# Kernel tuning notes

Hardware: AMD Instinct MI355X
Metric: run time of the kernel (lower is better)

The kernel has to match this reference:

```python
import jax, jax.numpy as jnp
import numpy as np

C_IN = 128
C_QK = C_IN // 8


def setup_inputs() -> dict:
    key = jax.random.key(0)
    kx, kq, kk, kv = jax.random.split(key, 4)
    x = jax.random.normal(kx, (8, C_IN, 64, 64), dtype=jnp.float32)
    # 1x1 conv weights, stored as (c_out, c_in); fan-in scaled init
    s = 1.0 / np.sqrt(C_IN)
    Wq = jax.random.normal(kq, (C_QK, C_IN), dtype=jnp.float32) * s
    Wk = jax.random.normal(kk, (C_QK, C_IN), dtype=jnp.float32) * s
    Wv = jax.random.normal(kv, (C_IN, C_IN), dtype=jnp.float32) * s
    gamma = jnp.ones((1,), dtype=jnp.float32) * 0.5  # nonzero so residual branch matters
    return {"x": x, "Wq": Wq, "Wk": Wk, "Wv": Wv, "gamma": gamma}


def reference(x, Wq, Wk, Wv, gamma):
    b, c, h, w = x.shape
    xt = rearr = x.reshape(b, c, h * w)            # b c n
    q = jnp.einsum('oc,bcn->bno', Wq, xt)          # b n c//8
    k = jnp.einsum('oc,bcn->bon', Wk, xt)          # b c//8 n
    v = jnp.einsum('oc,bcn->bno', Wv, xt)          # b n c
    energy = jnp.einsum('bno,bom->bnm', q, k)      # b n n (no scale, per source)
    attn = jax.nn.softmax(energy, axis=-1)
    out = jnp.einsum('bnm,bmc->bnc', attn, v)      # b n c
    out = out.transpose(0, 2, 1).reshape(b, c, h, w)
    return x + gamma[0] * out
```

## Files before the change

### kernel.cpp

```cpp
#include <hip/hip_runtime.h>
#include <hip/hip_bf16.h>


typedef __bf16 bf16x8 __attribute__((ext_vector_type(8)));
typedef __bf16 bf16x4 __attribute__((ext_vector_type(4)));
typedef float  f32x16 __attribute__((ext_vector_type(16)));

static constexpr int Bb = 8, Cc = 128, Nn = 4096, CQ = 16;

__device__ __forceinline__ f32x16 mfma32(bf16x8 a, bf16x8 b, f32x16 c) {
    return __builtin_amdgcn_mfma_f32_32x32x16_bf16(a, b, c, 0, 0, 0);
}
struct HL { __bf16 h, l; };
__device__ __forceinline__ HL hilo(float f) {
    HL r;
    r.h = (__bf16)f;
    r.l = (__bf16)(f - (float)r.h);
    return r;
}

__global__ __launch_bounds__(384) void qkv_kernel(
    const float* __restrict__ x, const float* __restrict__ Wq,
    const float* __restrict__ Wk, const float* __restrict__ Wv,
    __bf16* __restrict__ qw, __bf16* __restrict__ kw, __bf16* __restrict__ vw)
{
    const int b = blockIdx.y, tb = blockIdx.x, n0 = tb * 64, t = threadIdx.x;
    const int wave = t >> 6, lane = t & 63, lr = lane & 31, lq = lane >> 5;

    __shared__ __bf16 xh[64][136], xl[64][136];
    __shared__ __bf16 sc[4][32][40];

    if (t < 256) {
        const int n = lane, ci0 = (t >> 6) * 32;
        #pragma unroll
        for (int g = 0; g < 4; ++g) {
            float v[8];
            #pragma unroll
            for (int k = 0; k < 8; ++k)
                v[k] = x[((size_t)(b * Cc + ci0 + g * 8 + k)) * Nn + n0 + n];
            bf16x8 h8, l8;
            #pragma unroll
            for (int k = 0; k < 8; ++k) { HL z = hilo(v[k]); h8[k] = z.h; l8[k] = z.l; }
            *(bf16x8*)&xh[n][ci0 + g * 8] = h8;
            *(bf16x8*)&xl[n][ci0 + g * 8] = l8;
        }
    }
    __syncthreads();

    if (wave < 2) {
        const int nh = wave;
        const float* wrow = (lr < 16) ? (Wq + (size_t)lr * Cc)
                                      : (Wk + (size_t)(lr - 16) * Cc);
        f32x16 acc = {};
        #pragma unroll
        for (int ks = 0; ks < 8; ++ks) {
            float4 w0 = *(const float4*)(wrow + ks * 16 + lq * 8);
            float4 w1 = *(const float4*)(wrow + ks * 16 + lq * 8 + 4);
            bf16x8 ah, al;
            HL z;
            z = hilo(w0.x); ah[0] = z.h; al[0] = z.l;
            z = hilo(w0.y); ah[1] = z.h; al[1] = z.l;
            z = hilo(w0.z); ah[2] = z.h; al[2] = z.l;
            z = hilo(w0.w); ah[3] = z.h; al[3] = z.l;
            z = hilo(w1.x); ah[4] = z.h; al[4] = z.l;
            z = hilo(w1.y); ah[5] = z.h; al[5] = z.l;
            z = hilo(w1.z); ah[6] = z.h; al[6] = z.l;
            z = hilo(w1.w); ah[7] = z.h; al[7] = z.l;
            bf16x8 bh = *(const bf16x8*)&xh[nh * 32 + lr][ks * 16 + lq * 8];
            bf16x8 bl = *(const bf16x8*)&xl[nh * 32 + lr][ks * 16 + lq * 8];
            acc = mfma32(ah, bh, acc);
            acc = mfma32(al, bh, acc);
            acc = mfma32(ah, bl, acc);
        }
        const int tile = tb * 2 + nh;
        __bf16* qb = qw + (((size_t)b * 128 + tile) << 10);
        __bf16* kb = kw + (((size_t)b * 128 + tile) << 10);
        #pragma unroll
        for (int rg = 0; rg < 4; ++rg) {
            bf16x4 h4, l4;
            #pragma unroll
            for (int j = 0; j < 4; ++j) {
                float v = acc[rg * 4 + j];
                if (rg < 2) v *= 1.44269504089f;
                HL z = hilo(v);
                h4[j] = z.h; l4[j] = z.l;
            }
            const int off = (rg & 1) * 256 + lr * 8 + 4 * lq;
            __bf16* base = (rg < 2) ? qb : kb;
            *(bf16x4*)(base + off) = h4;
            *(bf16x4*)(base + 512 + off) = l4;
        }
    } else {
        const int ct = wave - 2;
        const int klr = (lr & ~12) | ((lr & 4) << 1) | ((lr & 8) >> 1);
        for (int nh = 0; nh < 2; ++nh) {
            f32x16 acc = {};
            #pragma unroll
            for (int ks = 0; ks < 8; ++ks) {
                const float* wp = Wv + (size_t)(ct * 32 + lr) * Cc + ks * 16 + lq * 8;
                float4 w0 = *(const float4*)wp;
                float4 w1 = *(const float4*)(wp + 4);
                bf16x8 a = { (__bf16)w0.x, (__bf16)w0.y, (__bf16)w0.z, (__bf16)w0.w,
                             (__bf16)w1.x, (__bf16)w1.y, (__bf16)w1.z, (__bf16)w1.w };
                bf16x8 bh = *(const bf16x8*)&xh[nh * 32 + lr][ks * 16 + lq * 8];
                acc = mfma32(a, bh, acc);
            }
            #pragma unroll
            for (int r = 0; r < 16; ++r) {
                int crow = (r & 3) + 8 * (r >> 2) + 4 * lq;
                sc[ct][crow][klr] = (__bf16)acc[r];
            }
            const int chunk = tb * 2 + nh;
            __bf16* vb = vw + (((size_t)b * 128 + chunk) << 12) + ct * 1024;
            #pragma unroll
            for (int u = 0; u < 2; ++u) {
                bf16x8 row = *(const bf16x8*)&sc[ct][lr][u * 16 + lq * 8];
                *(bf16x8*)(vb + u * 512 + lane * 8) = row;
            }
        }
    }
}

__global__ __launch_bounds__(256, 2) void attn_kernel(
    const float* __restrict__ x, const __bf16* __restrict__ qw,
    const __bf16* __restrict__ kw, const __bf16* __restrict__ vw,
    const float* __restrict__ gamma, float* __restrict__ out)
{
    const int h = blockIdx.x;
    const int b = h & 7;
    const int qt = h >> 3;
    const int t = threadIdx.x;
    const int wave = t >> 6, lane = t & 63, lr = lane & 31, lq = lane >> 5;
    const int kr = wave;

    __shared__ float accbuf[32][129];
    __shared__ float lbuf[32];

    const __bf16* qb = qw + (((size_t)b * 128 + qt) << 10) + lane * 8;
    const bf16x8 qhi = *(const bf16x8*)qb;
    const bf16x8 qlo = *(const bf16x8*)(qb + 512);

    const int c0 = kr * 32;
    const __bf16* kp = kw + (((size_t)b * 128 + c0) << 10) + lane * 8;
    const __bf16* vp = vw + (((size_t)b * 128 + c0) << 12) + lane * 8;

    f32x16 acc[4] = {{}, {}, {}, {}};
    float l_part = 0.f;

    bf16x8 akh = *(const bf16x8*)kp, akl = *(const bf16x8*)(kp + 512);
    bf16x8 av[8], bv[8];
    #pragma unroll
    for (int u = 0; u < 8; ++u) av[u] = *(const bf16x8*)(vp + u * 512);
    bf16x8 bkh, bkl;

    auto body = [&](const bf16x8& Kh, const bf16x8& Kl, const bf16x8 (&V)[8]) {
        f32x16 s = {};
        __builtin_amdgcn_s_setprio(1);
        s = mfma32(Kh, qhi, s);
        s = mfma32(Kl, qhi, s);
        s = mfma32(Kh, qlo, s);
        __builtin_amdgcn_s_setprio(0);

        float p[16];
        #pragma unroll
        for (int r = 0; r < 16; ++r) p[r] = __builtin_amdgcn_exp2f(s[r]);
        l_part += ((((p[0] + p[1]) + (p[2] + p[3])) + ((p[4] + p[5]) + (p[6] + p[7])))
                 + (((p[8] + p[9]) + (p[10] + p[11])) + ((p[12] + p[13]) + (p[14] + p[15]))));

        bf16x8 F0, F1;
        #pragma unroll
        for (int j = 0; j < 8; ++j) {
            F0[j] = (__bf16)p[j];
            F1[j] = (__bf16)p[8 + j];
        }

        __builtin_amdgcn_s_setprio(1);
        #pragma unroll
        for (int ct = 0; ct < 4; ++ct) {
            acc[ct] = mfma32(V[2 * ct],     F0, acc[ct]);
            acc[ct] = mfma32(V[2 * ct + 1], F1, acc[ct]);
        }
        __builtin_amdgcn_s_setprio(0);
    };

    for (int it = 0; it < 15; ++it) {
        kp += 1024; vp += 4096;
        bkh = *(const bf16x8*)kp; bkl = *(const bf16x8*)(kp + 512);
        #pragma unroll
        for (int u = 0; u < 8; ++u) bv[u] = *(const bf16x8*)(vp + u * 512);
        body(akh, akl, av);
        kp += 1024; vp += 4096;
        akh = *(const bf16x8*)kp; akl = *(const bf16x8*)(kp + 512);
        #pragma unroll
        for (int u = 0; u < 8; ++u) av[u] = *(const bf16x8*)(vp + u * 512);
        body(bkh, bkl, bv);
    }
    kp += 1024; vp += 4096;
    bkh = *(const bf16x8*)kp; bkl = *(const bf16x8*)(kp + 512);
    #pragma unroll
    for (int u = 0; u < 8; ++u) bv[u] = *(const bf16x8*)(vp + u * 512);
    body(akh, akl, av);
    body(bkh, bkl, bv);

    l_part += __shfl_xor(l_part, 32);

    if (kr == 0) {
        #pragma unroll
        for (int ct = 0; ct < 4; ++ct)
            #pragma unroll
            for (int r = 0; r < 16; ++r) {
                int c = (r & 3) + 8 * (r >> 2) + 4 * lq + 32 * ct;
                accbuf[lr][c] = acc[ct][r];
            }
        if (lane < 32) lbuf[lr] = l_part;
    }
    __syncthreads();
    if (kr != 0) {
        #pragma unroll
        for (int ct = 0; ct < 4; ++ct)
            #pragma unroll
            for (int r = 0; r < 16; ++r) {
                int c = (r & 3) + 8 * (r >> 2) + 4 * lq + 32 * ct;
                atomicAdd(&accbuf[lr][c], acc[ct][r]);
            }
        if (lane < 32) atomicAdd(&lbuf[lr], l_part);
    }
    __syncthreads();

    const float g = gamma[0];
    const int q = t & 31, cg = t >> 5;
    const float linv = 1.0f / lbuf[q];
    const int n0b = qt * 32;
    #pragma unroll
    for (int i = 0; i < 16; ++i) {
        int c = cg + 8 * i;
        size_t idx = ((size_t)(b * Cc + c)) * Nn + n0b + q;
        out[idx] = x[idx] + g * accbuf[q][c] * linv;
    }
}

extern "C" void kernel_launch(void* const* d_in, const int* in_sizes, int n_in,
                              void* d_out, int out_size, void* d_ws, size_t ws_size,
                              hipStream_t stream) {
    const float* x  = (const float*)d_in[0];
    const float* Wq = (const float*)d_in[1];
    const float* Wk = (const float*)d_in[2];
    const float* Wv = (const float*)d_in[3];
    const float* gm = (const float*)d_in[4];

    __bf16* qw = (__bf16*)d_ws;
    __bf16* kw = qw + (size_t)Bb * 128 * 1024;
    __bf16* vw = kw + (size_t)Bb * 128 * 1024;

    qkv_kernel<<<dim3(Nn / 64, Bb), 384, 0, stream>>>(x, Wq, Wk, Wv, qw, kw, vw);
    attn_kernel<<<dim3(Nn / 32 * Bb), 256, 0, stream>>>(x, qw, kw, vw, gm,
                                                        (float*)d_out);
}
```

Measured before the change: 187.4 us.

## Use persistent 512-thread attention blocks processing four query tiles each

The attention kernel now launches 256 blocks of 512 threads (one per CU) instead of 1024 blocks of 256 threads. Each block has two 4-wave halves, and each half handles two query tiles in sequence, reducing its partial results through a doubled shared-memory buffer. The aim is to cut block launch and tail overhead and to let the two halves share K/V reads through cache. The cost is fewer waves in flight per CU and extra block-wide barriers between tiles.

Result: slower. 213.1 us (+13.7%).

```diff
diff --git a/kernel.cpp b/kernel.cpp
--- a/kernel.cpp
+++ b/kernel.cpp
@@ -121,121 +121,133 @@
     }
 }
 
-__global__ __launch_bounds__(256, 2) void attn_kernel(
+__global__ __launch_bounds__(512, 2) void attn_kernel(
     const float* __restrict__ x, const __bf16* __restrict__ qw,
     const __bf16* __restrict__ kw, const __bf16* __restrict__ vw,
     const float* __restrict__ gamma, float* __restrict__ out)
 {
-    const int h = blockIdx.x;
-    const int b = h & 7;
-    const int qt = h >> 3;
+    const int i = blockIdx.x;
+    const int b = i & 7;
+    const int qt0 = (i >> 3) * 4;
     const int t = threadIdx.x;
     const int wave = t >> 6, lane = t & 63, lr = lane & 31, lq = lane >> 5;
-    const int kr = wave;
-
-    __shared__ float accbuf[32][129];
-    __shared__ float lbuf[32];
-
-    const __bf16* qb = qw + (((size_t)b * 128 + qt) << 10) + lane * 8;
-    const bf16x8 qhi = *(const bf16x8*)qb;
-    const bf16x8 qlo = *(const bf16x8*)(qb + 512);
-
+    const int kr = wave & 3, hh = wave >> 2;
+
+    __shared__ float accbuf[2][32][129];
+    __shared__ float lbuf[2][32];
+
+    const float g = gamma[0];
+    const __bf16* kwb = kw + (((size_t)b * 128) << 10);
+    const __bf16* vwb = vw + (((size_t)b * 128) << 12);
     const int c0 = kr * 32;
-    const __bf16* kp = kw + (((size_t)b * 128 + c0) << 10) + lane * 8;
-    const __bf16* vp = vw + (((size_t)b * 128 + c0) << 12) + lane * 8;
-
-    f32x16 acc[4] = {{}, {}, {}, {}};
-    float l_part = 0.f;
-
-    bf16x8 akh = *(const bf16x8*)kp, akl = *(const bf16x8*)(kp + 512);
-    bf16x8 av[8], bv[8];
-    #pragma unroll
-    for (int u = 0; u < 8; ++u) av[u] = *(const bf16x8*)(vp + u * 512);
-    bf16x8 bkh, bkl;
-
-    auto body = [&](const bf16x8& Kh, const bf16x8& Kl, const bf16x8 (&V)[8]) {
-        f32x16 s = {};
-        __builtin_amdgcn_s_setprio(1);
-        s = mfma32(Kh, qhi, s);
-        s = mfma32(Kl, qhi, s);
-        s = mfma32(Kh, qlo, s);
-        __builtin_amdgcn_s_setprio(0);
-
-        float p[16];
-        #pragma unroll
-        for (int r = 0; r < 16; ++r) p[r] = __builtin_amdgcn_exp2f(s[r]);
-        l_part += ((((p[0] + p[1]) + (p[2] + p[3])) + ((p[4] + p[5]) + (p[6] + p[7])))
-                 + (((p[8] + p[9]) + (p[10] + p[11])) + ((p[12] + p[13]) + (p[14] + p[15]))));
-
-        bf16x8 F0, F1;
-        #pragma unroll
-        for (int j = 0; j < 8; ++j) {
-            F0[j] = (__bf16)p[j];
-            F1[j] = (__bf16)p[8 + j];
-        }
-
-        __builtin_amdgcn_s_setprio(1);
-        #pragma unroll
-        for (int ct = 0; ct < 4; ++ct) {
-            acc[ct] = mfma32(V[2 * ct],     F0, acc[ct]);
-            acc[ct] = mfma32(V[2 * ct + 1], F1, acc[ct]);
-        }
-        __builtin_amdgcn_s_setprio(0);
-    };
-
-    for (int it = 0; it < 15; ++it) {
+
+    for (int u = 0; u < 2; ++u) {
+        const int qt = qt0 + u * 2 + hh;
+
+        const __bf16* qb = qw + (((size_t)b * 128 + qt) << 10) + lane * 8;
+        const bf16x8 qhi = *(const bf16x8*)qb;
+        const bf16x8 qlo = *(const bf16x8*)(qb + 512);
+
+        const __bf16* kp = kwb + ((size_t)c0 << 10) + lane * 8;
+        const __bf16* vp = vwb + ((size_t)c0 << 12) + lane * 8;
+
+        f32x16 acc[4] = {{}, {}, {}, {}};
+        float l_part = 0.f;
+
+        bf16x8 akh = *(const bf16x8*)kp, akl = *(const bf16x8*)(kp + 512);
+        bf16x8 av[8], bv[8];
+        #pragma unroll
+        for (int v8 = 0; v8 < 8; ++v8) av[v8] = *(const bf16x8*)(vp + v8 * 512);
+        bf16x8 bkh, bkl;
+
+        auto body = [&](const bf16x8& Kh, const bf16x8& Kl, const bf16x8 (&V)[8]) {
+            f32x16 s = {};
+            __builtin_amdgcn_s_setprio(1);
+            s = mfma32(Kh, qhi, s);
+            s = mfma32(Kl, qhi, s);
+            s = mfma32(Kh, qlo, s);
+            __builtin_amdgcn_s_setprio(0);
+
+            float p[16];
+            #pragma unroll
+            for (int r = 0; r < 16; ++r) p[r] = __builtin_amdgcn_exp2f(s[r]);
+            l_part += ((((p[0] + p[1]) + (p[2] + p[3])) + ((p[4] + p[5]) + (p[6] + p[7])))
+                     + (((p[8] + p[9]) + (p[10] + p[11])) + ((p[12] + p[13]) + (p[14] + p[15]))));
+
+            bf16x8 F0, F1;
+            #pragma unroll
+            for (int j = 0; j < 8; ++j) {
+                F0[j] = (__bf16)p[j];
+                F1[j] = (__bf16)p[8 + j];
+            }
+
+            __builtin_amdgcn_s_setprio(1);
+            #pragma unroll
+            for (int ct = 0; ct < 4; ++ct) {
+                acc[ct] = mfma32(V[2 * ct],     F0, acc[ct]);
+                acc[ct] = mfma32(V[2 * ct + 1], F1, acc[ct]);
+            }
+            __builtin_amdgcn_s_setprio(0);
+        };
+
+        for (int it = 0; it < 15; ++it) {
+            kp += 1024; vp += 4096;
+            bkh = *(const bf16x8*)kp; bkl = *(const bf16x8*)(kp + 512);
+            #pragma unroll
+            for (int v8 = 0; v8 < 8; ++v8) bv[v8] = *(const bf16x8*)(vp + v8 * 512);
+            body(akh, akl, av);
+            kp += 1024; vp += 4096;
+            akh = *(const bf16x8*)kp; akl = *(const bf16x8*)(kp + 512);
+            #pragma unroll
+            for (int v8 = 0; v8 < 8; ++v8) av[v8] = *(const bf16x8*)(vp + v8 * 512);
+            body(bkh, bkl, bv);
+        }
         kp += 1024; vp += 4096;
         bkh = *(const bf16x8*)kp; bkl = *(const bf16x8*)(kp + 512);
         #pragma unroll
-        for (int u = 0; u < 8; ++u) bv[u] = *(const bf16x8*)(vp + u * 512);
+        for (int v8 = 0; v8 < 8; ++v8) bv[v8] = *(const bf16x8*)(vp + v8 * 512);
         body(akh, akl, av);
-        kp += 1024; vp += 4096;
-        akh = *(const bf16x8*)kp; akl = *(const bf16x8*)(kp + 512);
-        #pragma unroll
-        for (int u = 0; u < 8; ++u) av[u] = *(const bf16x8*)(vp + u * 512);
         body(bkh, bkl, bv);
-    }
-    kp += 1024; vp += 4096;
-    bkh = *(const bf16x8*)kp; bkl = *(const bf16x8*)(kp + 512);
-    #pragma unroll
-    for (int u = 0; u < 8; ++u) bv[u] = *(const bf16x8*)(vp + u * 512);
-    body(akh, akl, av);
-    body(bkh, bkl, bv);
-
-    l_part += __shfl_xor(l_part, 32);
-
-    if (kr == 0) {
-        #pragma unroll
-        for (int ct = 0; ct < 4; ++ct)
-            #pragma unroll
-            for (int r = 0; r < 16; ++r) {
-                int c = (r & 3) + 8 * (r >> 2) + 4 * lq + 32 * ct;
-                accbuf[lr][c] = acc[ct][r];
-            }
-        if (lane < 32) lbuf[lr] = l_part;
-    }
-    __syncthreads();
-    if (kr != 0) {
-        #pragma unroll
-        for (int ct = 0; ct < 4; ++ct)
-            #pragma unroll
-            for (int r = 0; r < 16; ++r) {
-                int c = (r & 3) + 8 * (r >> 2) + 4 * lq + 32 * ct;
-                atomicAdd(&accbuf[lr][c], acc[ct][r]);
-            }
-        if (lane < 32) atomicAdd(&lbuf[lr], l_part);
-    }
-    __syncthreads();
-
-    const float g = gamma[0];
-    const int q = t & 31, cg = t >> 5;
-    const float linv = 1.0f / lbuf[q];
-    const int n0b = qt * 32;
-    #pragma unroll
-    for (int i = 0; i < 16; ++i) {
-        int c = cg + 8 * i;
-        size_t idx = ((size_t)(b * Cc + c)) * Nn + n0b + q;
-        out[idx] = x[idx] + g * accbuf[q][c] * linv;
+
+        l_part += __shfl_xor(l_part, 32);
+
+        if (kr == 0) {
+            #pragma unroll
+            for (int ct = 0; ct < 4; ++ct)
+                #pragma unroll
+                for (int r = 0; r < 16; ++r) {
+                    int c = (r & 3) + 8 * (r >> 2) + 4 * lq + 32 * ct;
+                    accbuf[hh][lr][c] = acc[ct][r];
+                }
+            if (lane < 32) lbuf[hh][lr] = l_part;
+        }
+        __syncthreads();
+        if (kr != 0) {
+            #pragma unroll
+            for (int ct = 0; ct < 4; ++ct)
+                #pragma unroll
+                for (int r = 0; r < 16; ++r) {
+                    int c = (r & 3) + 8 * (r >> 2) + 4 * lq + 32 * ct;
+                    atomicAdd(&accbuf[hh][lr][c], acc[ct][r]);
+                }
+            if (lane < 32) atomicAdd(&lbuf[hh][lr], l_part);
+        }
+        __syncthreads();
+
+        {
+            const int he = t >> 8;
+            const int tt = t & 255;
+            const int q = tt & 31, cg = tt >> 5;
+            const float linv = 1.0f / lbuf[he][q];
+            const int n0b = (qt0 + u * 2 + he) * 32;
+            #pragma unroll
+            for (int ii = 0; ii < 16; ++ii) {
+                int c = cg + 8 * ii;
+                size_t idx = ((size_t)(b * Cc + c)) * Nn + n0b + q;
+                out[idx] = x[idx] + g * accbuf[he][q][c] * linv;
+            }
+        }
+        __syncthreads();
     }
 }
 
@@ -253,6 +265,6 @@
     __bf16* vw = kw + (size_t)Bb * 128 * 1024;
 
     qkv_kernel<<<dim3(Nn / 64, Bb), 384, 0, stream>>>(x, Wq, Wk, Wv, qw, kw, vw);
-    attn_kernel<<<dim3(Nn / 32 * Bb), 256, 0, stream>>>(x, qw, kw, vw, gm,
-                                                        (float*)d_out);
-}
+    attn_kernel<<<dim3(256), 512, 0, stream>>>(x, qw, kw, vw, gm,
+                                               (float*)d_out);
+}
```
